# Kernel tuning notes

Hardware: AMD Instinct MI355X
Metric: run time of the kernel (lower is better)

The kernel has to match this reference:

```python
import jax, jax.numpy as jnp
import numpy as np

# Layer widths of the fixed ClassicPINN stack: 3 -> 8x7 -> 16x3 -> 32x3 -> 16 -> 3
WIDTHS = [3, 8, 8, 8, 8, 8, 8, 8, 16, 16, 16, 32, 32, 32, 16, 3]
N_LAYERS = 15
OUT_SIZES = [1, 1, 1]
N_POINTS = 1048576


def setup_inputs() -> dict:
    key = jax.random.key(0)
    ks = jax.random.split(key, 1 + 2 * N_LAYERS)
    inp = {"coords": jax.random.normal(ks[0], (N_POINTS, WIDTHS[0]), dtype=jnp.float32)}
    # PyTorch nn.Linear default init: U(-1/sqrt(fan_in), 1/sqrt(fan_in)) for W and b
    for i in range(N_LAYERS):
        fan_in, fan_out = WIDTHS[i], WIDTHS[i + 1]
        bound = 1.0 / np.sqrt(fan_in)
        inp[f"W{i}"] = jax.random.uniform(ks[1 + 2 * i], (fan_out, fan_in), jnp.float32, -bound, bound)
        inp[f"b{i}"] = jax.random.uniform(ks[2 + 2 * i], (fan_out,), jnp.float32, -bound, bound)
    return inp


def reference(coords, W0, W1, W2, W3, W4, W5, W6, W7, W8, W9, W10, W11, W12, W13, W14,
              b0, b1, b2, b3, b4, b5, b6, b7, b8, b9, b10, b11, b12, b13, b14):
    Ws = [W0, W1, W2, W3, W4, W5, W6, W7, W8, W9, W10, W11, W12, W13, W14]
    bs = [b0, b1, b2, b3, b4, b5, b6, b7, b8, b9, b10, b11, b12, b13, b14]
    h = coords  # [N, 3]
    for i in range(N_LAYERS):
        h = h @ Ws[i].T + bs[i]
        if i < N_LAYERS - 1:  # Tanh after every layer except the last
            h = jnp.tanh(h)
    # torch.split(output, [1,1,1], dim=1)
    return (h[:, 0:1], h[:, 1:2], h[:, 2:3])
```

## Files before the change

### kernel.cpp

```cpp
#include <hip/hip_runtime.h>


#define NPTS 1048576
#define P 2

struct PinnParams {
    const float* W[15];
    const float* B[15];
};

__device__ __forceinline__ float fast_tanh(float x) {
    x = fminf(fmaxf(x, -9.5f), 9.5f);
    float e = __builtin_amdgcn_exp2f(x * 2.8853900817779268f);
    return 1.0f - 2.0f * __builtin_amdgcn_rcpf(e + 1.0f);
}

template <int IN, int OUT, bool TANH>
__device__ __forceinline__ void layerP(const float* __restrict__ W,
                                       const float* __restrict__ B,
                                       const float (*h)[32], float (*o)[32]) {
    static_assert(IN % 4 == 0, "IN must be multiple of 4");
#pragma unroll
    for (int j = 0; j < OUT; ++j) {
        const float b = B[j];
        float acc[P];
#pragma unroll
        for (int p = 0; p < P; ++p) acc[p] = b;
#pragma unroll
        for (int k = 0; k < IN; k += 4) {
            const float4 w = *reinterpret_cast<const float4*>(W + j * IN + k);
#pragma unroll
            for (int p = 0; p < P; ++p) {
                acc[p] = fmaf(w.x, h[p][k + 0], acc[p]);
                acc[p] = fmaf(w.y, h[p][k + 1], acc[p]);
                acc[p] = fmaf(w.z, h[p][k + 2], acc[p]);
                acc[p] = fmaf(w.w, h[p][k + 3], acc[p]);
            }
        }
#pragma unroll
        for (int p = 0; p < P; ++p) o[p][j] = TANH ? fast_tanh(acc[p]) : acc[p];
    }
}

__device__ __forceinline__ void layer0(const float* __restrict__ W,
                                       const float* __restrict__ B,
                                       const float (*h)[32], float (*o)[32]) {
#pragma unroll
    for (int j = 0; j < 8; ++j) {
        const float w0 = W[3 * j + 0], w1 = W[3 * j + 1], w2 = W[3 * j + 2];
        const float b = B[j];
#pragma unroll
        for (int p = 0; p < P; ++p) {
            float acc = fmaf(w0, h[p][0], b);
            acc = fmaf(w1, h[p][1], acc);
            acc = fmaf(w2, h[p][2], acc);
            o[p][j] = fast_tanh(acc);
        }
    }
}

__global__ __launch_bounds__(256, 2) void pinn_fwd(const float* __restrict__ coords,
                                                   PinnParams prm,
                                                   float* __restrict__ out) {
    const int t = blockIdx.x * 256 + threadIdx.x;
    const int i0 = t * P;

    float a[P][32], c[P][32];
#pragma unroll
    for (int p = 0; p < P; ++p) {
        a[p][0] = coords[3 * (i0 + p) + 0];
        a[p][1] = coords[3 * (i0 + p) + 1];
        a[p][2] = coords[3 * (i0 + p) + 2];
    }

    layer0(prm.W[0], prm.B[0], a, c);
    layerP<8, 8, true>(prm.W[1], prm.B[1], c, a);
    layerP<8, 8, true>(prm.W[2], prm.B[2], a, c);
    layerP<8, 8, true>(prm.W[3], prm.B[3], c, a);
    layerP<8, 8, true>(prm.W[4], prm.B[4], a, c);
    layerP<8, 8, true>(prm.W[5], prm.B[5], c, a);
    layerP<8, 8, true>(prm.W[6], prm.B[6], a, c);
    layerP<8, 16, true>(prm.W[7], prm.B[7], c, a);
    layerP<16, 16, true>(prm.W[8], prm.B[8], a, c);
    layerP<16, 16, true>(prm.W[9], prm.B[9], c, a);
    layerP<16, 32, true>(prm.W[10], prm.B[10], a, c);
    layerP<32, 32, true>(prm.W[11], prm.B[11], c, a);
    layerP<32, 32, true>(prm.W[12], prm.B[12], a, c);
    layerP<32, 16, true>(prm.W[13], prm.B[13], c, a);
    layerP<16, 3, false>(prm.W[14], prm.B[14], a, c);

    *reinterpret_cast<float2*>(out + i0) = make_float2(c[0][0], c[1][0]);
    *reinterpret_cast<float2*>(out + NPTS + i0) = make_float2(c[0][1], c[1][1]);
    *reinterpret_cast<float2*>(out + 2 * NPTS + i0) = make_float2(c[0][2], c[1][2]);
}

extern "C" void kernel_launch(void* const* d_in, const int* in_sizes, int n_in,
                              void* d_out, int out_size, void* d_ws, size_t ws_size,
                              hipStream_t stream) {
    const float* coords = (const float*)d_in[0];
    PinnParams prm;
    for (int l = 0; l < 15; ++l) {
        prm.W[l] = (const float*)d_in[1 + 2 * l];
        prm.B[l] = (const float*)d_in[2 + 2 * l];
    }
    pinn_fwd<<<NPTS / (256 * P), 256, 0, stream>>>(coords, prm, (float*)d_out);
}
```

Measured before the change: 291.5 us.

## Stage weights in LDS and use packed f32x2 FMAs across point pairs

Copies all layer weights and biases into shared memory once per block, then reads them from LDS instead of through global/scalar loads. The two points per thread are held as 2-wide float vectors so the compiler can emit packed FMA instructions, and the coordinate load becomes three 8-byte vector loads. The clamp in tanh uses a single med3 instruction. This aims to raise FMA throughput, at the cost of an upfront per-block staging loop and barrier, and LDS reads that may replace scalar-register weight broadcasts.

```diff
diff --git a/kernel.cpp b/kernel.cpp
--- a/kernel.cpp
+++ b/kernel.cpp
@@ -4,94 +4,113 @@
 #define NPTS 1048576
 #define P 2
 
+typedef float f32x2 __attribute__((ext_vector_type(2)));
+
 struct PinnParams {
     const float* W[15];
     const float* B[15];
 };
 
+__constant__ constexpr int kIN[15]   = {3, 8, 8, 8, 8, 8, 8, 8, 16, 16, 16, 32, 32, 32, 16};
+__constant__ constexpr int kOUT[15]  = {8, 8, 8, 8, 8, 8, 8, 16, 16, 16, 32, 32, 32, 16, 3};
+__constant__ constexpr int kWSZ[15]  = {24, 64, 64, 64, 64, 64, 64, 128, 256, 256, 512, 1024, 1024, 512, 48};
+__constant__ constexpr int kWOFF[15] = {0, 24, 88, 152, 216, 280, 344, 408, 536, 792, 1048, 1560, 2584, 3608, 4120};
+__constant__ constexpr int kBOFF[15] = {0, 8, 16, 24, 32, 40, 48, 56, 72, 88, 104, 136, 168, 200, 216};
+#define WTOT 4168
+#define BTOT 219
+
 __device__ __forceinline__ float fast_tanh(float x) {
-    x = fminf(fmaxf(x, -9.5f), 9.5f);
+    x = __builtin_amdgcn_fmed3f(x, -9.5f, 9.5f);
     float e = __builtin_amdgcn_exp2f(x * 2.8853900817779268f);
     return 1.0f - 2.0f * __builtin_amdgcn_rcpf(e + 1.0f);
 }
 
-template <int IN, int OUT, bool TANH>
-__device__ __forceinline__ void layerP(const float* __restrict__ W,
-                                       const float* __restrict__ B,
-                                       const float (*h)[32], float (*o)[32]) {
-    static_assert(IN % 4 == 0, "IN must be multiple of 4");
+__device__ __forceinline__ f32x2 tanh2(f32x2 x) {
+    return f32x2{fast_tanh(x.x), fast_tanh(x.y)};
+}
+
+template <int L, bool TANH>
+__device__ __forceinline__ void layerL(const float* __restrict__ ldsw,
+                                       const float* __restrict__ ldsb,
+                                       const f32x2* h, f32x2* o) {
+    constexpr int IN = kIN[L], OUT = kOUT[L], WO = kWOFF[L], BO = kBOFF[L];
+    static_assert(IN % 4 == 0, "use layer0 for IN=3");
 #pragma unroll
     for (int j = 0; j < OUT; ++j) {
-        const float b = B[j];
-        float acc[P];
-#pragma unroll
-        for (int p = 0; p < P; ++p) acc[p] = b;
+        const float b = ldsb[BO + j];
+        f32x2 acc = {b, b};
 #pragma unroll
         for (int k = 0; k < IN; k += 4) {
-            const float4 w = *reinterpret_cast<const float4*>(W + j * IN + k);
-#pragma unroll
-            for (int p = 0; p < P; ++p) {
-                acc[p] = fmaf(w.x, h[p][k + 0], acc[p]);
-                acc[p] = fmaf(w.y, h[p][k + 1], acc[p]);
-                acc[p] = fmaf(w.z, h[p][k + 2], acc[p]);
-                acc[p] = fmaf(w.w, h[p][k + 3], acc[p]);
-            }
+            const float4 w = *reinterpret_cast<const float4*>(ldsw + WO + j * IN + k);
+            acc = __builtin_elementwise_fma(f32x2{w.x, w.x}, h[k + 0], acc);
+            acc = __builtin_elementwise_fma(f32x2{w.y, w.y}, h[k + 1], acc);
+            acc = __builtin_elementwise_fma(f32x2{w.z, w.z}, h[k + 2], acc);
+            acc = __builtin_elementwise_fma(f32x2{w.w, w.w}, h[k + 3], acc);
         }
-#pragma unroll
-        for (int p = 0; p < P; ++p) o[p][j] = TANH ? fast_tanh(acc[p]) : acc[p];
+        o[j] = TANH ? tanh2(acc) : acc;
     }
 }
 
-__device__ __forceinline__ void layer0(const float* __restrict__ W,
-                                       const float* __restrict__ B,
-                                       const float (*h)[32], float (*o)[32]) {
+__device__ __forceinline__ void layer0(const float* __restrict__ ldsw,
+                                       const float* __restrict__ ldsb,
+                                       const f32x2* h, f32x2* o) {
 #pragma unroll
     for (int j = 0; j < 8; ++j) {
-        const float w0 = W[3 * j + 0], w1 = W[3 * j + 1], w2 = W[3 * j + 2];
-        const float b = B[j];
-#pragma unroll
-        for (int p = 0; p < P; ++p) {
-            float acc = fmaf(w0, h[p][0], b);
-            acc = fmaf(w1, h[p][1], acc);
-            acc = fmaf(w2, h[p][2], acc);
-            o[p][j] = fast_tanh(acc);
-        }
+        const float w0 = ldsw[3 * j], w1 = ldsw[3 * j + 1], w2 = ldsw[3 * j + 2];
+        const float b = ldsb[j];
+        f32x2 acc = {b, b};
+        acc = __builtin_elementwise_fma(f32x2{w0, w0}, h[0], acc);
+        acc = __builtin_elementwise_fma(f32x2{w1, w1}, h[1], acc);
+        acc = __builtin_elementwise_fma(f32x2{w2, w2}, h[2], acc);
+        o[j] = tanh2(acc);
     }
 }
 
 __global__ __launch_bounds__(256, 2) void pinn_fwd(const float* __restrict__ coords,
                                                    PinnParams prm,
                                                    float* __restrict__ out) {
-    const int t = blockIdx.x * 256 + threadIdx.x;
+    __shared__ __align__(16) float ldsw[WTOT];
+    __shared__ float ldsb[BTOT];
+
+    const int tid = threadIdx.x;
+#pragma unroll
+    for (int l = 0; l < 15; ++l) {
+        const float* __restrict__ W = prm.W[l];
+        for (int idx = tid; idx < kWSZ[l]; idx += 256) ldsw[kWOFF[l] + idx] = W[idx];
+        const float* __restrict__ B = prm.B[l];
+        if (tid < kOUT[l]) ldsb[kBOFF[l] + tid] = B[tid];
+    }
+    __syncthreads();
+
+    const int t = blockIdx.x * 256 + tid;
     const int i0 = t * P;
+    const f32x2* cp = reinterpret_cast<const f32x2*>(coords + 3 * i0);
+    const f32x2 q0 = cp[0], q1 = cp[1], q2 = cp[2];
 
-    float a[P][32], c[P][32];
-#pragma unroll
-    for (int p = 0; p < P; ++p) {
-        a[p][0] = coords[3 * (i0 + p) + 0];
-        a[p][1] = coords[3 * (i0 + p) + 1];
-        a[p][2] = coords[3 * (i0 + p) + 2];
-    }
+    f32x2 a[32], c[32];
+    a[0] = f32x2{q0.x, q1.y};
+    a[1] = f32x2{q0.y, q2.x};
+    a[2] = f32x2{q1.x, q2.y};
 
-    layer0(prm.W[0], prm.B[0], a, c);
-    layerP<8, 8, true>(prm.W[1], prm.B[1], c, a);
-    layerP<8, 8, true>(prm.W[2], prm.B[2], a, c);
-    layerP<8, 8, true>(prm.W[3], prm.B[3], c, a);
-    layerP<8, 8, true>(prm.W[4], prm.B[4], a, c);
-    layerP<8, 8, true>(prm.W[5], prm.B[5], c, a);
-    layerP<8, 8, true>(prm.W[6], prm.B[6], a, c);
-    layerP<8, 16, true>(prm.W[7], prm.B[7], c, a);
-    layerP<16, 16, true>(prm.W[8], prm.B[8], a, c);
-    layerP<16, 16, true>(prm.W[9], prm.B[9], c, a);
-    layerP<16, 32, true>(prm.W[10], prm.B[10], a, c);
-    layerP<32, 32, true>(prm.W[11], prm.B[11], c, a);
-    layerP<32, 32, true>(prm.W[12], prm.B[12], a, c);
-    layerP<32, 16, true>(prm.W[13], prm.B[13], c, a);
-    layerP<16, 3, false>(prm.W[14], prm.B[14], a, c);
+    layer0(ldsw, ldsb, a, c);
+    layerL<1, true>(ldsw, ldsb, c, a);
+    layerL<2, true>(ldsw, ldsb, a, c);
+    layerL<3, true>(ldsw, ldsb, c, a);
+    layerL<4, true>(ldsw, ldsb, a, c);
+    layerL<5, true>(ldsw, ldsb, c, a);
+    layerL<6, true>(ldsw, ldsb, a, c);
+    layerL<7, true>(ldsw, ldsb, c, a);
+    layerL<8, true>(ldsw, ldsb, a, c);
+    layerL<9, true>(ldsw, ldsb, c, a);
+    layerL<10, true>(ldsw, ldsb, a, c);
+    layerL<11, true>(ldsw, ldsb, c, a);
+    layerL<12, true>(ldsw, ldsb, a, c);
+    layerL<13, true>(ldsw, ldsb, c, a);
+    layerL<14, false>(ldsw, ldsb, a, c);
 
-    *reinterpret_cast<float2*>(out + i0) = make_float2(c[0][0], c[1][0]);
-    *reinterpret_cast<float2*>(out + NPTS + i0) = make_float2(c[0][1], c[1][1]);
-    *reinterpret_cast<float2*>(out + 2 * NPTS + i0) = make_float2(c[0][2], c[1][2]);
+    *reinterpret_cast<f32x2*>(out + i0) = c[0];
+    *reinterpret_cast<f32x2*>(out + NPTS + i0) = c[1];
+    *reinterpret_cast<f32x2*>(out + 2 * NPTS + i0) = c[2];
 }
 
 extern "C" void kernel_launch(void* const* d_in, const int* in_sizes, int n_in,
```

New measurement: 275.5 us. 5.5% less time.

## Use packed FMA along the K dimension with one point per thread

Applied to the files above, without the earlier changes.

Each thread now handles one point instead of two. Activations are stored as float2 vectors and multiplied with float2 weight pairs through elementwise FMA, so the compiler can emit packed v_pk_fma_f32 instructions; the two partial sums are added at the end of each output. The launch bound is raised to 6 blocks per CU and the grid is doubled. The tanh clamp now uses fmed3. The risks are an extra horizontal add per output, less reuse of each weight load across points, and possible register spilling at the higher occupancy target.

```diff
diff --git a/kernel.cpp b/kernel.cpp
--- a/kernel.cpp
+++ b/kernel.cpp
@@ -2,7 +2,8 @@
 
 
 #define NPTS 1048576
-#define P 2
+
+typedef float f32x2 __attribute__((ext_vector_type(2)));
 
 struct PinnParams {
     const float* W[15];
@@ -10,88 +11,88 @@
 };
 
 __device__ __forceinline__ float fast_tanh(float x) {
-    x = fminf(fmaxf(x, -9.5f), 9.5f);
+    x = __builtin_amdgcn_fmed3f(x, -9.5f, 9.5f);
     float e = __builtin_amdgcn_exp2f(x * 2.8853900817779268f);
     return 1.0f - 2.0f * __builtin_amdgcn_rcpf(e + 1.0f);
 }
 
 template <int IN, int OUT, bool TANH>
-__device__ __forceinline__ void layerP(const float* __restrict__ W,
+__device__ __forceinline__ void layerK(const float* __restrict__ W,
                                        const float* __restrict__ B,
-                                       const float (*h)[32], float (*o)[32]) {
-    static_assert(IN % 4 == 0, "IN must be multiple of 4");
+                                       const f32x2* h2, f32x2* o2) {
+    static_assert(IN % 2 == 0 && OUT % 2 == 0, "");
 #pragma unroll
     for (int j = 0; j < OUT; ++j) {
-        const float b = B[j];
-        float acc[P];
+        f32x2 acc = {B[j], 0.0f};
 #pragma unroll
-        for (int p = 0; p < P; ++p) acc[p] = b;
-#pragma unroll
-        for (int k = 0; k < IN; k += 4) {
-            const float4 w = *reinterpret_cast<const float4*>(W + j * IN + k);
-#pragma unroll
-            for (int p = 0; p < P; ++p) {
-                acc[p] = fmaf(w.x, h[p][k + 0], acc[p]);
-                acc[p] = fmaf(w.y, h[p][k + 1], acc[p]);
-                acc[p] = fmaf(w.z, h[p][k + 2], acc[p]);
-                acc[p] = fmaf(w.w, h[p][k + 3], acc[p]);
-            }
+        for (int k2 = 0; k2 < IN / 2; ++k2) {
+            const f32x2 w = *reinterpret_cast<const f32x2*>(W + j * IN + 2 * k2);
+            acc = __builtin_elementwise_fma(w, h2[k2], acc);
         }
-#pragma unroll
-        for (int p = 0; p < P; ++p) o[p][j] = TANH ? fast_tanh(acc[p]) : acc[p];
+        const float s = acc.x + acc.y;
+        const float r = TANH ? fast_tanh(s) : s;
+        if (j & 1) o2[j >> 1].y = r; else o2[j >> 1].x = r;
     }
 }
 
 __device__ __forceinline__ void layer0(const float* __restrict__ W,
                                        const float* __restrict__ B,
-                                       const float (*h)[32], float (*o)[32]) {
+                                       float h0, float h1, float h2v, f32x2* o2) {
 #pragma unroll
     for (int j = 0; j < 8; ++j) {
-        const float w0 = W[3 * j + 0], w1 = W[3 * j + 1], w2 = W[3 * j + 2];
-        const float b = B[j];
-#pragma unroll
-        for (int p = 0; p < P; ++p) {
-            float acc = fmaf(w0, h[p][0], b);
-            acc = fmaf(w1, h[p][1], acc);
-            acc = fmaf(w2, h[p][2], acc);
-            o[p][j] = fast_tanh(acc);
-        }
+        float s = fmaf(W[3 * j + 0], h0, B[j]);
+        s = fmaf(W[3 * j + 1], h1, s);
+        s = fmaf(W[3 * j + 2], h2v, s);
+        const float r = fast_tanh(s);
+        if (j & 1) o2[j >> 1].y = r; else o2[j >> 1].x = r;
     }
 }
 
-__global__ __launch_bounds__(256, 2) void pinn_fwd(const float* __restrict__ coords,
+__device__ __forceinline__ void layer14(const float* __restrict__ W,
+                                        const float* __restrict__ B,
+                                        const f32x2* h2, float* o) {
+#pragma unroll
+    for (int j = 0; j < 3; ++j) {
+        f32x2 acc = {B[j], 0.0f};
+#pragma unroll
+        for (int k2 = 0; k2 < 8; ++k2) {
+            const f32x2 w = *reinterpret_cast<const f32x2*>(W + j * 16 + 2 * k2);
+            acc = __builtin_elementwise_fma(w, h2[k2], acc);
+        }
+        o[j] = acc.x + acc.y;
+    }
+}
+
+__global__ __launch_bounds__(256, 6) void pinn_fwd(const float* __restrict__ coords,
                                                    PinnParams prm,
                                                    float* __restrict__ out) {
     const int t = blockIdx.x * 256 + threadIdx.x;
-    const int i0 = t * P;
 
-    float a[P][32], c[P][32];
-#pragma unroll
-    for (int p = 0; p < P; ++p) {
-        a[p][0] = coords[3 * (i0 + p) + 0];
-        a[p][1] = coords[3 * (i0 + p) + 1];
-        a[p][2] = coords[3 * (i0 + p) + 2];
-    }
+    f32x2 a2[16], c2[16];
+    const float x = coords[3 * t + 0];
+    const float y = coords[3 * t + 1];
+    const float z = coords[3 * t + 2];
 
-    layer0(prm.W[0], prm.B[0], a, c);
-    layerP<8, 8, true>(prm.W[1], prm.B[1], c, a);
-    layerP<8, 8, true>(prm.W[2], prm.B[2], a, c);
-    layerP<8, 8, true>(prm.W[3], prm.B[3], c, a);
-    layerP<8, 8, true>(prm.W[4], prm.B[4], a, c);
-    layerP<8, 8, true>(prm.W[5], prm.B[5], c, a);
-    layerP<8, 8, true>(prm.W[6], prm.B[6], a, c);
-    layerP<8, 16, true>(prm.W[7], prm.B[7], c, a);
-    layerP<16, 16, true>(prm.W[8], prm.B[8], a, c);
-    layerP<16, 16, true>(prm.W[9], prm.B[9], c, a);
-    layerP<16, 32, true>(prm.W[10], prm.B[10], a, c);
-    layerP<32, 32, true>(prm.W[11], prm.B[11], c, a);
-    layerP<32, 32, true>(prm.W[12], prm.B[12], a, c);
-    layerP<32, 16, true>(prm.W[13], prm.B[13], c, a);
-    layerP<16, 3, false>(prm.W[14], prm.B[14], a, c);
+    layer0(prm.W[0], prm.B[0], x, y, z, a2);
+    layerK<8, 8, true>(prm.W[1], prm.B[1], a2, c2);
+    layerK<8, 8, true>(prm.W[2], prm.B[2], c2, a2);
+    layerK<8, 8, true>(prm.W[3], prm.B[3], a2, c2);
+    layerK<8, 8, true>(prm.W[4], prm.B[4], c2, a2);
+    layerK<8, 8, true>(prm.W[5], prm.B[5], a2, c2);
+    layerK<8, 8, true>(prm.W[6], prm.B[6], c2, a2);
+    layerK<8, 16, true>(prm.W[7], prm.B[7], a2, c2);
+    layerK<16, 16, true>(prm.W[8], prm.B[8], c2, a2);
+    layerK<16, 16, true>(prm.W[9], prm.B[9], a2, c2);
+    layerK<16, 32, true>(prm.W[10], prm.B[10], c2, a2);
+    layerK<32, 32, true>(prm.W[11], prm.B[11], a2, c2);
+    layerK<32, 32, true>(prm.W[12], prm.B[12], c2, a2);
+    layerK<32, 16, true>(prm.W[13], prm.B[13], a2, c2);
+    float o[3];
+    layer14(prm.W[14], prm.B[14], c2, o);
 
-    *reinterpret_cast<float2*>(out + i0) = make_float2(c[0][0], c[1][0]);
-    *reinterpret_cast<float2*>(out + NPTS + i0) = make_float2(c[0][1], c[1][1]);
-    *reinterpret_cast<float2*>(out + 2 * NPTS + i0) = make_float2(c[0][2], c[1][2]);
+    out[t] = o[0];
+    out[NPTS + t] = o[1];
+    out[2 * NPTS + t] = o[2];
 }
 
 extern "C" void kernel_launch(void* const* d_in, const int* in_sizes, int n_in,
@@ -103,5 +104,5 @@
         prm.W[l] = (const float*)d_in[1 + 2 * l];
         prm.B[l] = (const float*)d_in[2 + 2 * l];
     }
-    pinn_fwd<<<NPTS / (256 * P), 256, 0, stream>>>(coords, prm, (float*)d_out);
+    pinn_fwd<<<NPTS / 256, 256, 0, stream>>>(coords, prm, (float*)d_out);
 }
```

New measurement: 243.2 us. -16.6%, faster.
